# Kernel optimization log

Measured on AMD Instinct MI355X. Metric: run time of the kernel, lower is better.

## Reference

```python
import jax, jax.numpy as jnp
import numpy as np

B, S, HID = 8, 4096, 1024
NH, HD = 16, 64  # heads, head_dim
LN_EPS = 1e-12


def setup_inputs() -> dict:
    key = jax.random.key(0)
    ks = jax.random.split(key, 12)
    sd = 1.0 / np.sqrt(HID)
    return {
        "input_tensor": jax.random.normal(ks[0], (B, S, HID), jnp.float32),
        "attention_mask": jnp.ones((B, S), jnp.int32),
        "ln_gamma": jnp.ones((HID,), jnp.float32),
        "ln_beta": jnp.zeros((HID,), jnp.float32),
        "Wq": jax.random.normal(ks[1], (HID, HID), jnp.float32) * sd,
        "bq": jnp.zeros((HID,), jnp.float32),
        "Wk": jax.random.normal(ks[2], (HID, HID), jnp.float32) * sd,
        "bk": jnp.zeros((HID,), jnp.float32),
        "Wv": jax.random.normal(ks[3], (HID, HID), jnp.float32) * sd,
        "bv": jnp.zeros((HID,), jnp.float32),
        "Wo": jax.random.normal(ks[4], (HID, HID), jnp.float32) * sd,
        "bo": jnp.zeros((HID,), jnp.float32),
    }


def _layernorm(x, g, b):
    mu = jnp.mean(x, axis=-1, keepdims=True)
    var = jnp.mean(jnp.square(x - mu), axis=-1, keepdims=True)
    return (x - mu) * jax.lax.rsqrt(var + LN_EPS) * g + b


def reference(input_tensor, attention_mask, ln_gamma, ln_beta,
              Wq, bq, Wk, bk, Wv, bv, Wo, bo):
    # NOTE: attention_mask is accepted but unused, matching the original module.
    x = input_tensor
    x_norm = _layernorm(x, ln_gamma, ln_beta)
    # projections: query from normalized input, key/value from raw input
    q = (x_norm @ Wq.T + bq).reshape(B, S, NH, HD).transpose(0, 2, 1, 3)  # bhsd
    k = (x @ Wk.T + bk).reshape(B, S, NH, HD).transpose(0, 2, 1, 3)      # bhsd
    v = (x @ Wv.T + bv).reshape(B, S, NH, HD).transpose(0, 2, 1, 3)      # bhsd

    eq = jax.nn.elu(q)
    ek = jax.nn.elu(k)
    # per-token L2 norms over head_dim (matches norm over d in both layouts)
    eq = eq / jnp.linalg.norm(eq, axis=-1, keepdims=True)
    ek = ek / jnp.linalg.norm(ek, axis=-1, keepdims=True)

    # linear attention: Q (K^T V), never materializing [S,S]
    kv = jnp.einsum('bhsd,bhse->bhde', ek, v)          # [B,H,d,d]
    ctx = jnp.einsum('bhsd,bhde->bhse', eq, kv) / np.sqrt(HD)

    ctx = ctx.transpose(0, 2, 1, 3).reshape(B, S, HID)
    out = ctx @ Wo.T + bo
    return out + x  # residual (dropouts are identity in eval mode)
```

## Files before the change

kernel.cpp:

```cpp
#include <hip/hip_runtime.h>

typedef unsigned short u16;
typedef unsigned int   u32;
typedef __attribute__((ext_vector_type(8))) __bf16 bf16x8;
typedef __attribute__((ext_vector_type(4))) float  f32x4;

#define BQ   8
#define SQ   4096
#define NHQ  16
#define HIDD 1024
#define TOKN 32768

__device__ __forceinline__ u16 f2bf(float f){
  u32 u = __builtin_bit_cast(u32, f);
  u += 0x7fffu + ((u >> 16) & 1u);
  return (u16)(u >> 16);
}
__device__ __forceinline__ float bf2f(u16 h){
  return __builtin_bit_cast(float, (u32)h << 16);
}
__device__ __forceinline__ void gl16(const void* g, void* l){
  __builtin_amdgcn_global_load_lds((const __attribute__((address_space(1))) void*)g,
                                   (__attribute__((address_space(3))) void*)l, 16, 0, 0);
}
#define MFMA(a,b,c) __builtin_amdgcn_mfma_f32_16x16x32_bf16((a),(b),(c),0,0,0)

__global__ __launch_bounds__(256) void k_cast4(const float* __restrict__ wq,
    const float* __restrict__ wk, const float* __restrict__ wv, const float* __restrict__ wo,
    u16* __restrict__ oq, u16* __restrict__ okv, u16* __restrict__ oo){
  const int sel = blockIdx.x >> 10;
  const int i = ((blockIdx.x & 1023) << 8) + threadIdx.x;
  const float* in = (sel == 0) ? wq : (sel == 1) ? wk : (sel == 2) ? wv : wo;
  u16* o = (sel == 0) ? oq : (sel == 1) ? okv : (sel == 2) ? (okv + 1024 * 1024) : oo;
  float4 v = ((const float4*)in)[i];
  ushort4 r;
  r.x = f2bf(v.x); r.y = f2bf(v.y); r.z = f2bf(v.z); r.w = f2bf(v.w);
  ((ushort4*)o)[i] = r;
}

__global__ __launch_bounds__(256) void k_ln(const float* __restrict__ x, const float* __restrict__ g,
    const float* __restrict__ be, u16* __restrict__ xbf, u16* __restrict__ xnbf){
  const int row = blockIdx.x, t = threadIdx.x;
  const float4 v = ((const float4*)(x + (size_t)row * HIDD))[t];
  float s  = v.x + v.y + v.z + v.w;
  float ss = v.x*v.x + v.y*v.y + v.z*v.z + v.w*v.w;
  #pragma unroll
  for (int o = 1; o < 64; o <<= 1){ s += __shfl_xor(s, o); ss += __shfl_xor(ss, o); }
  __shared__ float sm[8];
  const int lane = t & 63, wid = t >> 6;
  if (lane == 0){ sm[wid] = s; sm[wid + 4] = ss; }
  __syncthreads();
  s  = sm[0] + sm[1] + sm[2] + sm[3];
  ss = sm[4] + sm[5] + sm[6] + sm[7];
  const float mu   = s * (1.f / 1024.f);
  const float var  = ss * (1.f / 1024.f) - mu * mu;
  const float rstd = rsqrtf(var + 1e-12f);
  const float4 gg = ((const float4*)g)[t];
  const float4 bb = ((const float4*)be)[t];
  ushort4 xo, no;
  xo.x = f2bf(v.x); no.x = f2bf((v.x - mu) * rstd * gg.x + bb.x);
  xo.y = f2bf(v.y); no.y = f2bf((v.y - mu) * rstd * gg.y + bb.y);
  xo.z = f2bf(v.z); no.z = f2bf((v.z - mu) * rstd * gg.z + bb.z);
  xo.w = f2bf(v.w); no.w = f2bf((v.w - mu) * rstd * gg.w + bb.w);
  ((ushort4*)(xbf  + (size_t)row * HIDD))[t] = xo;
  ((ushort4*)(xnbf + (size_t)row * HIDD))[t] = no;
}

struct GP {
  const u16* A; const u16* W; const float* b1; const float* b2;
  int nsplit, lgNB, LDC, nblk; u16* outb;
};

template<int RES>
__global__ __launch_bounds__(512, 2) void k_gemm256(GP p0, GP p1, int seg0,
    const float* __restrict__ resid, float* __restrict__ outf){
  __shared__ union {
    u16 st[2][2][16384];
    float cep[8][1056];
  } sm;

  const GP& p = (blockIdx.x < seg0) ? p0 : p1;
  const int bseg = (blockIdx.x < seg0) ? blockIdx.x : blockIdx.x - seg0;
  const u16* __restrict__ A = p.A;
  const u16* __restrict__ W = p.W;
  const int lgNB = p.lgNB, LDC = p.LDC;

  const int wg = ((bseg & 7) * (p.nblk >> 3)) + (bseg >> 3);
  const int m0 = (wg >> lgNB) << 8;
  const int n0 = (wg & ((1 << lgNB) - 1)) << 8;

  const int t = threadIdx.x, lane = t & 63, wid = t >> 6;
  const int ln15 = lane & 15, hi = lane >> 4;
  const int wr = wid >> 2, wc = wid & 3;
  const int lg = lane & 7, lr = lane >> 3;

  auto stage = [&](int buf, int op, const u16* __restrict__ src, int rowoff, int kt){
    #pragma unroll
    for (int i = 0; i < 4; i++){
      const int cb  = ((i << 3) + wid) << 6;
      const int row = (cb >> 3) + lr;
      const int g   = lg ^ lr;
      gl16(src + (size_t)(rowoff + row) * HIDD + (kt << 6) + (g << 3),
           &sm.st[buf][op][cb << 3]);
    }
  };
  #define RD_A(c,m,ks) (*(const bf16x8*)&sm.st[c][0][(((wr << 7) + ((m) << 4) + ln15) << 6) + \
      (((((ks) << 2) + hi) ^ (lane & 7)) << 3)])
  #define RD_B(c,n,ks) (*(const bf16x8*)&sm.st[c][1][(((wc << 6) + ((n) << 4) + ln15) << 6) + \
      (((((ks) << 2) + hi) ^ (lane & 7)) << 3)])

  f32x4 acc[8][4] = {};

  stage(0, 0, A, m0, 0);
  stage(0, 1, W, n0, 0);
  stage(1, 1, W, n0, 1);
  asm volatile("s_waitcnt vmcnt(4)" ::: "memory");
  __builtin_amdgcn_s_barrier();
  asm volatile("" ::: "memory");

  const int NT = HIDD / 64;
  for (int kt = 0; kt < NT; ++kt){
    const int c = kt & 1;
    bf16x8 af[4][2], bq[4][2];
    #pragma unroll
    for (int m = 0; m < 4; m++){ af[m][0] = RD_A(c, m, 0); af[m][1] = RD_A(c, m, 1); }
    #pragma unroll
    for (int n = 0; n < 4; n++){ bq[n][0] = RD_B(c, n, 0); bq[n][1] = RD_B(c, n, 1); }
    const int ka = kt + 1 < NT ? kt + 1 : NT - 1;
    stage(c ^ 1, 0, A, m0, ka);
    __builtin_amdgcn_s_setprio(1);
    #pragma unroll
    for (int m = 0; m < 4; m++)
      #pragma unroll
      for (int n = 0; n < 4; n++){
        acc[m][n] = MFMA(af[m][0], bq[n][0], acc[m][n]);
        acc[m][n] = MFMA(af[m][1], bq[n][1], acc[m][n]);
      }
    __builtin_amdgcn_s_setprio(0);
    asm volatile("" ::: "memory");
    __builtin_amdgcn_s_barrier();
    asm volatile("" ::: "memory");
    #pragma unroll
    for (int m = 0; m < 4; m++){ af[m][0] = RD_A(c, m + 4, 0); af[m][1] = RD_A(c, m + 4, 1); }
    const int kb = kt + 2 < NT ? kt + 2 : NT - 1;
    stage(c, 1, W, n0, kb);
    __builtin_amdgcn_s_setprio(1);
    #pragma unroll
    for (int m = 0; m < 4; m++)
      #pragma unroll
      for (int n = 0; n < 4; n++){
        acc[m + 4][n] = MFMA(af[m][0], bq[n][0], acc[m + 4][n]);
        acc[m + 4][n] = MFMA(af[m][1], bq[n][1], acc[m + 4][n]);
      }
    __builtin_amdgcn_s_setprio(0);
    asm volatile("s_waitcnt vmcnt(4)" ::: "memory");
    __builtin_amdgcn_s_barrier();
    asm volatile("" ::: "memory");
  }
  #undef RD_A
  #undef RD_B

  asm volatile("s_waitcnt vmcnt(0)" ::: "memory");
  __builtin_amdgcn_s_barrier();
  asm volatile("" ::: "memory");

  const float* bp = (n0 < p.nsplit) ? p.b1 : (p.b2 - p.nsplit);
  float bn[4];
  #pragma unroll
  for (int n = 0; n < 4; n++) bn[n] = bp[n0 + (wc << 6) + (n << 4) + ln15];

  float* cw = &sm.cep[wid][0];
  const int rr = lane >> 3, cb8 = (lane & 7) << 3;

  if constexpr (RES){
    #pragma unroll
    for (int m = 0; m < 8; m++){
      #pragma unroll
      for (int n = 0; n < 4; n++)
        #pragma unroll
        for (int r = 0; r < 4; r++)
          cw[((hi << 2) + r) * 66 + (n << 4) + ln15] = acc[m][n][r] + bn[n];
      #pragma unroll
      for (int j = 0; j < 2; j++){
        const int row = (j << 3) + rr;
        const size_t gr = (size_t)(m0 + (wr << 7) + (m << 4) + row);
        const size_t gidx = gr * LDC + n0 + (wc << 6) + cb8;
        const size_t ridx = gr * HIDD + n0 + (wc << 6) + cb8;
        const float4 ra = *(const float4*)&resid[ridx];
        const float4 rb = *(const float4*)&resid[ridx + 4];
        float4 o0, o1;
        o0.x = cw[row * 66 + cb8 + 0] + ra.x;
        o0.y = cw[row * 66 + cb8 + 1] + ra.y;
        o0.z = cw[row * 66 + cb8 + 2] + ra.z;
        o0.w = cw[row * 66 + cb8 + 3] + ra.w;
        o1.x = cw[row * 66 + cb8 + 4] + rb.x;
        o1.y = cw[row * 66 + cb8 + 5] + rb.y;
        o1.z = cw[row * 66 + cb8 + 6] + rb.z;
        o1.w = cw[row * 66 + cb8 + 7] + rb.w;
        *(float4*)&outf[gidx]     = o0;
        *(float4*)&outf[gidx + 4] = o1;
      }
    }
  } else {
    u16* outb = p.outb;
    #pragma unroll
    for (int m = 0; m < 8; m++){
      #pragma unroll
      for (int n = 0; n < 4; n++)
        #pragma unroll
        for (int r = 0; r < 4; r++)
          cw[((hi << 2) + r) * 66 + (n << 4) + ln15] = acc[m][n][r] + bn[n];
      #pragma unroll
      for (int j = 0; j < 2; j++){
        const int row = (j << 3) + rr;
        u32 ro[4];
        #pragma unroll
        for (int pq = 0; pq < 4; pq++){
          float v0 = cw[row * 66 + cb8 + 2 * pq];
          float v1 = cw[row * 66 + cb8 + 2 * pq + 1];
          ro[pq] = (u32)f2bf(v0) | ((u32)f2bf(v1) << 16);
        }
        uint4 o; o.x = ro[0]; o.y = ro[1]; o.z = ro[2]; o.w = ro[3];
        *(uint4*)&outb[(size_t)(m0 + (wr << 7) + (m << 4) + row) * LDC
                       + n0 + (wc << 6) + cb8] = o;
      }
    }
  }
}

__global__ __launch_bounds__(256) void k_transpose2(const u16* __restrict__ kvb,
                                                    u16* __restrict__ ekT, u16* __restrict__ vT){
  __shared__ float tile[64][65];
  __shared__ float pr[64][4];
  __shared__ float rn[64];
  const int sb = blockIdx.x << 6, h2 = blockIdx.y, b = blockIdx.z;
  const int h = h2 & 15;
  const int isK = (h2 >> 4) == 0;
  const u16* in = kvb + ((h2 >> 4) << 10);
  u16* outp = isK ? ekT : vT;
  const int t = threadIdx.x;
  {
    const int tok = t >> 2, q = t & 3;
    const u16* src = in + (size_t)(b * SQ + sb + tok) * 2048 + (h << 6) + (q << 4);
    uint4 u0 = *(const uint4*)src;
    uint4 u1 = *(const uint4*)(src + 8);
    u32 uu[8] = {u0.x, u0.y, u0.z, u0.w, u1.x, u1.y, u1.z, u1.w};
    float ss = 0.f;
    #pragma unroll
    for (int i = 0; i < 8; i++){
      float f0 = bf2f((u16)(uu[i] & 0xffff));
      float f1 = bf2f((u16)(uu[i] >> 16));
      if (isK){
        f0 = f0 > 0.f ? f0 : expm1f(f0);
        f1 = f1 > 0.f ? f1 : expm1f(f1);
        ss += f0 * f0 + f1 * f1;
      }
      tile[tok][(q << 4) + 2*i]     = f0;
      tile[tok][(q << 4) + 2*i + 1] = f1;
    }
    if (isK) pr[tok][q] = ss;
  }
  __syncthreads();
  if (isK){
    if (t < 64) rn[t] = rsqrtf(pr[t][0] + pr[t][1] + pr[t][2] + pr[t][3]);
    __syncthreads();
  }
  const int d = t >> 2, sq2 = (t & 3) << 4;
  u16* dst = outp + ((size_t)(b * NHQ + h) * 64 + d) * SQ + sb + sq2;
  u32 ro[8];
  #pragma unroll
  for (int i = 0; i < 8; i++){
    float v0 = tile[sq2 + 2*i][d];
    float v1 = tile[sq2 + 2*i + 1][d];
    if (isK){ v0 *= rn[sq2 + 2*i]; v1 *= rn[sq2 + 2*i + 1]; }
    ro[i] = (u32)f2bf(v0) | ((u32)f2bf(v1) << 16);
  }
  uint4 o0; o0.x = ro[0]; o0.y = ro[1]; o0.z = ro[2]; o0.w = ro[3];
  uint4 o1; o1.x = ro[4]; o1.y = ro[5]; o1.z = ro[6]; o1.w = ro[7];
  *(uint4*)dst = o0;
  *(uint4*)(dst + 8) = o1;
}

__global__ __launch_bounds__(256) void k_kv(const u16* __restrict__ vT, const u16* __restrict__ ekT,
                                            u16* __restrict__ kvT){
  const int bh = blockIdx.x;
  const u16* Av = vT  + (size_t)bh * 64 * SQ;
  const u16* Bk = ekT + (size_t)bh * 64 * SQ;
  const int lane = threadIdx.x & 63, wid = threadIdx.x >> 6;
  const int ln15 = lane & 15, hi = lane >> 4;
  f32x4 acc[4][4] = {};
  const int kb = wid << 10;
  for (int ks = 0; ks < 32; ++ks){
    const int k0 = kb + (ks << 5) + (hi << 3);
    bf16x8 af[4], bfr[4];
    #pragma unroll
    for (int m = 0; m < 4; m++) af[m]  = *(const bf16x8*)(Av + (size_t)((m << 4) + ln15) * SQ + k0);
    #pragma unroll
    for (int n = 0; n < 4; n++) bfr[n] = *(const bf16x8*)(Bk + (size_t)((n << 4) + ln15) * SQ + k0);
    #pragma unroll
    for (int m = 0; m < 4; m++)
      #pragma unroll
      for (int n = 0; n < 4; n++)
        acc[m][n] = MFMA(af[m], bfr[n], acc[m][n]);
  }
  __shared__ float red[64][64];
  for (int w = 0; w < 4; ++w){
    if (wid == w){
      #pragma unroll
      for (int m = 0; m < 4; m++)
        #pragma unroll
        for (int n = 0; n < 4; n++)
          #pragma unroll
          for (int r = 0; r < 4; r++){
            int row = (m << 4) + (hi << 2) + r;
            int col = (n << 4) + ln15;
            if (w == 0) red[row][col] = acc[m][n][r];
            else        red[row][col] += acc[m][n][r];
          }
    }
    __syncthreads();
  }
  u16* dst = kvT + (size_t)bh * 4096;
  const int tt = threadIdx.x;
  #pragma unroll
  for (int i = 0; i < 16; i++){
    int idx = tt * 16 + i;
    dst[idx] = f2bf(red[idx >> 6][idx & 63] * 0.125f);
  }
}

__global__ __launch_bounds__(256) void k_ctx(const u16* __restrict__ q, const u16* __restrict__ kvT,
                                             u16* __restrict__ ctx){
  __shared__ u16 Alds[1024 * 8];
  __shared__ u16 Blds[512 * 8];
  __shared__ float prn[128][2];
  const int sb = blockIdx.x << 7;
  const int h = blockIdx.y, b = blockIdx.z;
  const int bh = (b << 4) + h;
  const int t = threadIdx.x, lane = t & 63, wid = t >> 6;
  const int ln15 = lane & 15, hi = lane >> 4;
  {
    uint4 va[4]; uint4 vb[2];
    #pragma unroll
    for (int i = 0; i < 4; i++){
      int c = (wid << 6) + (i << 8) + lane;
      int g = c >> 7, row = c & 127;
      va[i] = *(const uint4*)(q + (size_t)(b * SQ + sb + row) * HIDD + (h << 6) + g * 8);
    }
    #pragma unroll
    for (int i = 0; i < 2; i++){
      int c = (wid << 6) + (i << 8) + lane;
      int g = c >> 6, row = c & 63;
      vb[i] = *(const uint4*)(kvT + (size_t)bh * 4096 + (row << 6) + g * 8);
    }
    #pragma unroll
    for (int i = 0; i < 4; i++)
      *(uint4*)&Alds[((wid << 6) + (i << 8) + lane) * 8] = va[i];
    #pragma unroll
    for (int i = 0; i < 2; i++)
      *(uint4*)&Blds[((wid << 6) + (i << 8) + lane) * 8] = vb[i];
  }
  __syncthreads();
  {
    const int row = t & 127, half = t >> 7;
    float vals[4][8]; float ss = 0.f;
    #pragma unroll
    for (int g4 = 0; g4 < 4; g4++){
      const int g = (half << 2) + g4;
      uint4 u = *(const uint4*)&Alds[((g << 7) + row) * 8];
      u32 uu[4] = {u.x, u.y, u.z, u.w};
      #pragma unroll
      for (int i = 0; i < 4; i++){
        float f0 = bf2f((u16)(uu[i] & 0xffff));
        float f1 = bf2f((u16)(uu[i] >> 16));
        f0 = f0 > 0.f ? f0 : expm1f(f0);
        f1 = f1 > 0.f ? f1 : expm1f(f1);
        vals[g4][2*i] = f0; vals[g4][2*i+1] = f1;
        ss += f0 * f0 + f1 * f1;
      }
    }
    prn[row][half] = ss;
    __syncthreads();
    const float rn = rsqrtf(prn[row][0] + prn[row][1]);
    #pragma unroll
    for (int g4 = 0; g4 < 4; g4++){
      const int g = (half << 2) + g4;
      u32 ro[4];
      #pragma unroll
      for (int i = 0; i < 4; i++)
        ro[i] = (u32)f2bf(vals[g4][2*i] * rn) | ((u32)f2bf(vals[g4][2*i+1] * rn) << 16);
      uint4 o; o.x = ro[0]; o.y = ro[1]; o.z = ro[2]; o.w = ro[3];
      *(uint4*)&Alds[((g << 7) + row) * 8] = o;
    }
  }
  __syncthreads();
  f32x4 acc[2][4] = {};
  #pragma unroll
  for (int k2 = 0; k2 < 2; k2++){
    const int g = (k2 << 2) + hi;
    bf16x8 af[2], bfr[4];
    #pragma unroll
    for (int m = 0; m < 2; m++) af[m]  = *(const bf16x8*)&Alds[((g << 7) + (wid << 5) + (m << 4) + ln15) * 8];
    #pragma unroll
    for (int n = 0; n < 4; n++) bfr[n] = *(const bf16x8*)&Blds[((g << 6) + (n << 4) + ln15) * 8];
    #pragma unroll
    for (int m = 0; m < 2; m++)
      #pragma unroll
      for (int n = 0; n < 4; n++)
        acc[m][n] = MFMA(af[m], bfr[n], acc[m][n]);
  }
  #pragma unroll
  for (int m = 0; m < 2; m++)
    #pragma unroll
    for (int n = 0; n < 4; n++)
      #pragma unroll
      for (int r = 0; r < 4; r++){
        int srow = sb + (wid << 5) + (m << 4) + (hi << 2) + r;
        int col  = (n << 4) + ln15;
        ctx[(size_t)(b * SQ + srow) * HIDD + (h << 6) + col] = f2bf(acc[m][n][r]);
      }
}

extern "C" void kernel_launch(void* const* d_in, const int* in_sizes, int n_in,
                              void* d_out, int out_size, void* d_ws, size_t ws_size,
                              hipStream_t stream){
  const float* x   = (const float*)d_in[0];
  const float* lng = (const float*)d_in[2];
  const float* lnb = (const float*)d_in[3];
  const float* Wq  = (const float*)d_in[4];
  const float* bq  = (const float*)d_in[5];
  const float* Wk  = (const float*)d_in[6];
  const float* bk  = (const float*)d_in[7];
  const float* Wv  = (const float*)d_in[8];
  const float* bv  = (const float*)d_in[9];
  const float* Wo  = (const float*)d_in[10];
  const float* bo  = (const float*)d_in[11];
  float* out = (float*)d_out;

  char* w = (char*)d_ws;
  const size_t MB = 1ull << 20;
  u16* wqb  = (u16*)(w + 0   * MB);
  u16* wkvb = (u16*)(w + 2   * MB);
  u16* wob  = (u16*)(w + 6   * MB);
  u16* xbf  = (u16*)(w + 8   * MB);
  u16* xnbf = (u16*)(w + 72  * MB);
  u16* qb   = (u16*)(w + 136 * MB);
  u16* kvb  = (u16*)(w + 200 * MB);
  u16* kvT  = (u16*)(w + 328 * MB);
  u16* ekT = xnbf;
  u16* vT  = xbf;
  u16* ctx = kvb;

  k_cast4<<<4096, 256, 0, stream>>>(Wq, Wk, Wv, Wo, wqb, wkvb, wob);
  k_ln<<<TOKN, 256, 0, stream>>>(x, lng, lnb, xbf, xnbf);

  GP pq  = { xnbf, wqb,  bq, bq, 1 << 30, 2, 1024, 512,  qb  };
  GP pkv = { xbf,  wkvb, bk, bv, 1024,    3, 2048, 1024, kvb };
  k_gemm256<0><<<1536, 512, 0, stream>>>(pq, pkv, 512, nullptr, nullptr);

  k_transpose2<<<dim3(64, 32, 8), 256, 0, stream>>>(kvb, ekT, vT);
  k_kv<<<128, 256, 0, stream>>>(vT, ekT, kvT);
  k_ctx<<<dim3(32, 16, 8), 256, 0, stream>>>(qb, kvT, ctx);

  GP po = { ctx, wob, bo, bo, 1 << 30, 2, 1024, 512, nullptr };
  k_gemm256<1><<<512, 512, 0, stream>>>(po, po, 512, x, out);

  (void)in_sizes; (void)n_in; (void)out_size; (void)ws_size;
}
```

Measured before the change: 693.0 us.

## Write V transposed from QKV GEMM epilogue and split output GEMM pipeline finer

The QKV GEMM epilogue now writes the V half directly in transposed [b,h,d,s] layout, so the separate transpose kernel only handles K (elu plus normalize). This drops one full read and write of V through global memory. The output-projection GEMM also switches to a variant that issues A/B staging in quarter steps, with four barriers per k-tile instead of two. That adds synchronization overhead in exchange for interleaving loads more finely with MFMA work.

```diff
diff --git a/kernel.cpp b/kernel.cpp
--- a/kernel.cpp
+++ b/kernel.cpp
@@ -68,15 +68,16 @@
 
 struct GP {
   const u16* A; const u16* W; const float* b1; const float* b2;
-  int nsplit, lgNB, LDC, nblk; u16* outb;
+  int nsplit, lgNB, LDC, nblk; u16* outb; u16* voutT;
 };
 
-template<int RES>
+template<int RES, int SPLIT>
 __global__ __launch_bounds__(512, 2) void k_gemm256(GP p0, GP p1, int seg0,
     const float* __restrict__ resid, float* __restrict__ outf){
   __shared__ union {
     u16 st[2][2][16384];
     float cep[8][1056];
+    float cep2[8][2112];
   } sm;
 
   const GP& p = (blockIdx.x < seg0) ? p0 : p1;
@@ -104,10 +105,22 @@
            &sm.st[buf][op][cb << 3]);
     }
   };
+  auto stageH = [&](int buf, int op, const u16* __restrict__ src, int rowoff, int kt, int half){
+    #pragma unroll
+    for (int i2 = 0; i2 < 2; i2++){
+      const int i = (half << 1) + i2;
+      const int cb  = ((i << 3) + wid) << 6;
+      const int row = (cb >> 3) + lr;
+      const int g   = lg ^ lr;
+      gl16(src + (size_t)(rowoff + row) * HIDD + (kt << 6) + (g << 3),
+           &sm.st[buf][op][cb << 3]);
+    }
+  };
   #define RD_A(c,m,ks) (*(const bf16x8*)&sm.st[c][0][(((wr << 7) + ((m) << 4) + ln15) << 6) + \
       (((((ks) << 2) + hi) ^ (lane & 7)) << 3)])
   #define RD_B(c,n,ks) (*(const bf16x8*)&sm.st[c][1][(((wc << 6) + ((n) << 4) + ln15) << 6) + \
       (((((ks) << 2) + hi) ^ (lane & 7)) << 3)])
+  #define BARF do { asm volatile("" ::: "memory"); __builtin_amdgcn_s_barrier(); asm volatile("" ::: "memory"); } while(0)
 
   f32x4 acc[8][4] = {};
 
@@ -115,64 +128,122 @@
   stage(0, 1, W, n0, 0);
   stage(1, 1, W, n0, 1);
   asm volatile("s_waitcnt vmcnt(4)" ::: "memory");
-  __builtin_amdgcn_s_barrier();
-  asm volatile("" ::: "memory");
+  BARF;
 
   const int NT = HIDD / 64;
-  for (int kt = 0; kt < NT; ++kt){
-    const int c = kt & 1;
-    bf16x8 af[4][2], bq[4][2];
-    #pragma unroll
-    for (int m = 0; m < 4; m++){ af[m][0] = RD_A(c, m, 0); af[m][1] = RD_A(c, m, 1); }
-    #pragma unroll
-    for (int n = 0; n < 4; n++){ bq[n][0] = RD_B(c, n, 0); bq[n][1] = RD_B(c, n, 1); }
-    const int ka = kt + 1 < NT ? kt + 1 : NT - 1;
-    stage(c ^ 1, 0, A, m0, ka);
-    __builtin_amdgcn_s_setprio(1);
-    #pragma unroll
-    for (int m = 0; m < 4; m++)
-      #pragma unroll
-      for (int n = 0; n < 4; n++){
-        acc[m][n] = MFMA(af[m][0], bq[n][0], acc[m][n]);
-        acc[m][n] = MFMA(af[m][1], bq[n][1], acc[m][n]);
-      }
-    __builtin_amdgcn_s_setprio(0);
-    asm volatile("" ::: "memory");
-    __builtin_amdgcn_s_barrier();
-    asm volatile("" ::: "memory");
-    #pragma unroll
-    for (int m = 0; m < 4; m++){ af[m][0] = RD_A(c, m + 4, 0); af[m][1] = RD_A(c, m + 4, 1); }
-    const int kb = kt + 2 < NT ? kt + 2 : NT - 1;
-    stage(c, 1, W, n0, kb);
-    __builtin_amdgcn_s_setprio(1);
-    #pragma unroll
-    for (int m = 0; m < 4; m++)
-      #pragma unroll
-      for (int n = 0; n < 4; n++){
-        acc[m + 4][n] = MFMA(af[m][0], bq[n][0], acc[m + 4][n]);
-        acc[m + 4][n] = MFMA(af[m][1], bq[n][1], acc[m + 4][n]);
-      }
-    __builtin_amdgcn_s_setprio(0);
-    asm volatile("s_waitcnt vmcnt(4)" ::: "memory");
-    __builtin_amdgcn_s_barrier();
-    asm volatile("" ::: "memory");
+  if constexpr (SPLIT == 0){
+    for (int kt = 0; kt < NT; ++kt){
+      const int c = kt & 1;
+      bf16x8 af[4][2], bq[4][2];
+      #pragma unroll
+      for (int m = 0; m < 4; m++){ af[m][0] = RD_A(c, m, 0); af[m][1] = RD_A(c, m, 1); }
+      #pragma unroll
+      for (int n = 0; n < 4; n++){ bq[n][0] = RD_B(c, n, 0); bq[n][1] = RD_B(c, n, 1); }
+      const int ka = kt + 1 < NT ? kt + 1 : NT - 1;
+      stage(c ^ 1, 0, A, m0, ka);
+      __builtin_amdgcn_s_setprio(1);
+      #pragma unroll
+      for (int m = 0; m < 4; m++)
+        #pragma unroll
+        for (int n = 0; n < 4; n++){
+          acc[m][n] = MFMA(af[m][0], bq[n][0], acc[m][n]);
+          acc[m][n] = MFMA(af[m][1], bq[n][1], acc[m][n]);
+        }
+      __builtin_amdgcn_s_setprio(0);
+      BARF;
+      #pragma unroll
+      for (int m = 0; m < 4; m++){ af[m][0] = RD_A(c, m + 4, 0); af[m][1] = RD_A(c, m + 4, 1); }
+      const int kb = kt + 2 < NT ? kt + 2 : NT - 1;
+      stage(c, 1, W, n0, kb);
+      __builtin_amdgcn_s_setprio(1);
+      #pragma unroll
+      for (int m = 0; m < 4; m++)
+        #pragma unroll
+        for (int n = 0; n < 4; n++){
+          acc[m + 4][n] = MFMA(af[m][0], bq[n][0], acc[m + 4][n]);
+          acc[m + 4][n] = MFMA(af[m][1], bq[n][1], acc[m + 4][n]);
+        }
+      __builtin_amdgcn_s_setprio(0);
+      asm volatile("s_waitcnt vmcnt(4)" ::: "memory");
+      BARF;
+    }
+  } else {
+    for (int kt = 0; kt < NT; ++kt){
+      const int c = kt & 1;
+      const int ka  = kt + 1 < NT ? kt + 1 : NT - 1;
+      const int kb2 = kt + 2 < NT ? kt + 2 : NT - 1;
+      bf16x8 af[2][2], bq[4][2];
+      af[0][0] = RD_A(c, 0, 0); af[0][1] = RD_A(c, 0, 1);
+      af[1][0] = RD_A(c, 1, 0); af[1][1] = RD_A(c, 1, 1);
+      #pragma unroll
+      for (int n = 0; n < 4; n++){ bq[n][0] = RD_B(c, n, 0); bq[n][1] = RD_B(c, n, 1); }
+      stageH(c ^ 1, 0, A, m0, ka, 0);
+      __builtin_amdgcn_s_setprio(1);
+      #pragma unroll
+      for (int m = 0; m < 2; m++)
+        #pragma unroll
+        for (int n = 0; n < 4; n++){
+          acc[m][n] = MFMA(af[m][0], bq[n][0], acc[m][n]);
+          acc[m][n] = MFMA(af[m][1], bq[n][1], acc[m][n]);
+        }
+      __builtin_amdgcn_s_setprio(0);
+      BARF;
+      af[0][0] = RD_A(c, 2, 0); af[0][1] = RD_A(c, 2, 1);
+      af[1][0] = RD_A(c, 3, 0); af[1][1] = RD_A(c, 3, 1);
+      stageH(c ^ 1, 0, A, m0, ka, 1);
+      __builtin_amdgcn_s_setprio(1);
+      #pragma unroll
+      for (int m = 0; m < 2; m++)
+        #pragma unroll
+        for (int n = 0; n < 4; n++){
+          acc[m + 2][n] = MFMA(af[m][0], bq[n][0], acc[m + 2][n]);
+          acc[m + 2][n] = MFMA(af[m][1], bq[n][1], acc[m + 2][n]);
+        }
+      __builtin_amdgcn_s_setprio(0);
+      BARF;
+      af[0][0] = RD_A(c, 4, 0); af[0][1] = RD_A(c, 4, 1);
+      af[1][0] = RD_A(c, 5, 0); af[1][1] = RD_A(c, 5, 1);
+      stageH(c, 1, W, n0, kb2, 0);
+      __builtin_amdgcn_s_setprio(1);
+      #pragma unroll
+      for (int m = 0; m < 2; m++)
+        #pragma unroll
+        for (int n = 0; n < 4; n++){
+          acc[m + 4][n] = MFMA(af[m][0], bq[n][0], acc[m + 4][n]);
+          acc[m + 4][n] = MFMA(af[m][1], bq[n][1], acc[m + 4][n]);
+        }
+      __builtin_amdgcn_s_setprio(0);
+      BARF;
+      af[0][0] = RD_A(c, 6, 0); af[0][1] = RD_A(c, 6, 1);
+      af[1][0] = RD_A(c, 7, 0); af[1][1] = RD_A(c, 7, 1);
+      stageH(c, 1, W, n0, kb2, 1);
+      __builtin_amdgcn_s_setprio(1);
+      #pragma unroll
+      for (int m = 0; m < 2; m++)
+        #pragma unroll
+        for (int n = 0; n < 4; n++){
+          acc[m + 6][n] = MFMA(af[m][0], bq[n][0], acc[m + 6][n]);
+          acc[m + 6][n] = MFMA(af[m][1], bq[n][1], acc[m + 6][n]);
+        }
+      __builtin_amdgcn_s_setprio(0);
+      asm volatile("s_waitcnt vmcnt(4)" ::: "memory");
+      BARF;
+    }
   }
   #undef RD_A
   #undef RD_B
 
   asm volatile("s_waitcnt vmcnt(0)" ::: "memory");
-  __builtin_amdgcn_s_barrier();
-  asm volatile("" ::: "memory");
+  BARF;
 
   const float* bp = (n0 < p.nsplit) ? p.b1 : (p.b2 - p.nsplit);
   float bn[4];
   #pragma unroll
   for (int n = 0; n < 4; n++) bn[n] = bp[n0 + (wc << 6) + (n << 4) + ln15];
 
-  float* cw = &sm.cep[wid][0];
-  const int rr = lane >> 3, cb8 = (lane & 7) << 3;
-
   if constexpr (RES){
+    float* cw = &sm.cep[wid][0];
+    const int rr = lane >> 3, cb8 = (lane & 7) << 3;
     #pragma unroll
     for (int m = 0; m < 8; m++){
       #pragma unroll
@@ -201,7 +272,41 @@
         *(float4*)&outf[gidx + 4] = o1;
       }
     }
+  } else if (p.voutT != nullptr && n0 >= p.nsplit){
+    float* cw = &sm.cep2[wid][0];
+    const int e0 = n0 - p.nsplit + (wc << 6);
+    const int hh = e0 >> 6;
+    u16* vt = p.voutT;
+    #pragma unroll
+    for (int mp = 0; mp < 4; mp++){
+      #pragma unroll
+      for (int mh = 0; mh < 2; mh++){
+        const int m = (mp << 1) + mh;
+        #pragma unroll
+        for (int n = 0; n < 4; n++)
+          #pragma unroll
+          for (int r = 0; r < 4; r++)
+            cw[((mh << 4) + (hi << 2) + r) * 66 + (n << 4) + ln15] = acc[m][n][r] + bn[n];
+      }
+      const int rg0 = m0 + (wr << 7) + (mp << 5);
+      const int bb = rg0 >> 12, s0 = rg0 & 4095;
+      u16* dst = vt + (((size_t)(bb << 4) + hh) * 64 + lane) * SQ + s0;
+      #pragma unroll
+      for (int j = 0; j < 4; j++){
+        u32 ro[4];
+        #pragma unroll
+        for (int q = 0; q < 4; q++){
+          float v0 = cw[((j << 3) + 2 * q    ) * 66 + lane];
+          float v1 = cw[((j << 3) + 2 * q + 1) * 66 + lane];
+          ro[q] = (u32)f2bf(v0) | ((u32)f2bf(v1) << 16);
+        }
+        uint4 o; o.x = ro[0]; o.y = ro[1]; o.z = ro[2]; o.w = ro[3];
+        *(uint4*)&dst[j << 3] = o;
+      }
+    }
   } else {
+    float* cw = &sm.cep[wid][0];
+    const int rr = lane >> 3, cb8 = (lane & 7) << 3;
     u16* outb = p.outb;
     #pragma unroll
     for (int m = 0; m < 8; m++){
@@ -226,22 +331,19 @@
       }
     }
   }
-}
-
-__global__ __launch_bounds__(256) void k_transpose2(const u16* __restrict__ kvb,
-                                                    u16* __restrict__ ekT, u16* __restrict__ vT){
+  #undef BARF
+}
+
+__global__ __launch_bounds__(256) void k_transposeK(const u16* __restrict__ kb,
+                                                    u16* __restrict__ ekT){
   __shared__ float tile[64][65];
   __shared__ float pr[64][4];
   __shared__ float rn[64];
-  const int sb = blockIdx.x << 6, h2 = blockIdx.y, b = blockIdx.z;
-  const int h = h2 & 15;
-  const int isK = (h2 >> 4) == 0;
-  const u16* in = kvb + ((h2 >> 4) << 10);
-  u16* outp = isK ? ekT : vT;
+  const int sb = blockIdx.x << 6, h = blockIdx.y, b = blockIdx.z;
   const int t = threadIdx.x;
   {
     const int tok = t >> 2, q = t & 3;
-    const u16* src = in + (size_t)(b * SQ + sb + tok) * 2048 + (h << 6) + (q << 4);
+    const u16* src = kb + (size_t)(b * SQ + sb + tok) * 1024 + (h << 6) + (q << 4);
     uint4 u0 = *(const uint4*)src;
     uint4 u1 = *(const uint4*)(src + 8);
     u32 uu[8] = {u0.x, u0.y, u0.z, u0.w, u1.x, u1.y, u1.z, u1.w};
@@ -250,29 +352,24 @@
     for (int i = 0; i < 8; i++){
       float f0 = bf2f((u16)(uu[i] & 0xffff));
       float f1 = bf2f((u16)(uu[i] >> 16));
-      if (isK){
-        f0 = f0 > 0.f ? f0 : expm1f(f0);
-        f1 = f1 > 0.f ? f1 : expm1f(f1);
-        ss += f0 * f0 + f1 * f1;
-      }
+      f0 = f0 > 0.f ? f0 : expm1f(f0);
+      f1 = f1 > 0.f ? f1 : expm1f(f1);
+      ss += f0 * f0 + f1 * f1;
       tile[tok][(q << 4) + 2*i]     = f0;
       tile[tok][(q << 4) + 2*i + 1] = f1;
     }
-    if (isK) pr[tok][q] = ss;
+    pr[tok][q] = ss;
   }
   __syncthreads();
-  if (isK){
-    if (t < 64) rn[t] = rsqrtf(pr[t][0] + pr[t][1] + pr[t][2] + pr[t][3]);
-    __syncthreads();
-  }
+  if (t < 64) rn[t] = rsqrtf(pr[t][0] + pr[t][1] + pr[t][2] + pr[t][3]);
+  __syncthreads();
   const int d = t >> 2, sq2 = (t & 3) << 4;
-  u16* dst = outp + ((size_t)(b * NHQ + h) * 64 + d) * SQ + sb + sq2;
+  u16* dst = ekT + ((size_t)(b * NHQ + h) * 64 + d) * SQ + sb + sq2;
   u32 ro[8];
   #pragma unroll
   for (int i = 0; i < 8; i++){
-    float v0 = tile[sq2 + 2*i][d];
-    float v1 = tile[sq2 + 2*i + 1][d];
-    if (isK){ v0 *= rn[sq2 + 2*i]; v1 *= rn[sq2 + 2*i + 1]; }
+    float v0 = tile[sq2 + 2*i][d]     * rn[sq2 + 2*i];
+    float v1 = tile[sq2 + 2*i + 1][d] * rn[sq2 + 2*i + 1];
     ro[i] = (u32)f2bf(v0) | ((u32)f2bf(v1) << 16);
   }
   uint4 o0; o0.x = ro[0]; o0.y = ro[1]; o0.z = ro[2]; o0.w = ro[3];
@@ -445,25 +542,25 @@
   u16* xbf  = (u16*)(w + 8   * MB);
   u16* xnbf = (u16*)(w + 72  * MB);
   u16* qb   = (u16*)(w + 136 * MB);
-  u16* kvb  = (u16*)(w + 200 * MB);
+  u16* kb   = (u16*)(w + 200 * MB);
+  u16* vT   = (u16*)(w + 264 * MB);
   u16* kvT  = (u16*)(w + 328 * MB);
   u16* ekT = xnbf;
-  u16* vT  = xbf;
-  u16* ctx = kvb;
+  u16* ctx = kb;
 
   k_cast4<<<4096, 256, 0, stream>>>(Wq, Wk, Wv, Wo, wqb, wkvb, wob);
   k_ln<<<TOKN, 256, 0, stream>>>(x, lng, lnb, xbf, xnbf);
 
-  GP pq  = { xnbf, wqb,  bq, bq, 1 << 30, 2, 1024, 512,  qb  };
-  GP pkv = { xbf,  wkvb, bk, bv, 1024,    3, 2048, 1024, kvb };
-  k_gemm256<0><<<1536, 512, 0, stream>>>(pq, pkv, 512, nullptr, nullptr);
-
-  k_transpose2<<<dim3(64, 32, 8), 256, 0, stream>>>(kvb, ekT, vT);
+  GP pq  = { xnbf, wqb,  bq, bq, 1 << 30, 2, 1024, 512,  qb, nullptr };
+  GP pkv = { xbf,  wkvb, bk, bv, 1024,    3, 1024, 1024, kb, vT };
+  k_gemm256<0, 0><<<1536, 512, 0, stream>>>(pq, pkv, 512, nullptr, nullptr);
+
+  k_transposeK<<<dim3(64, 16, 8), 256, 0, stream>>>(kb, ekT);
   k_kv<<<128, 256, 0, stream>>>(vT, ekT, kvT);
   k_ctx<<<dim3(32, 16, 8), 256, 0, stream>>>(qb, kvT, ctx);
 
-  GP po = { ctx, wob, bo, bo, 1 << 30, 2, 1024, 512, nullptr };
-  k_gemm256<1><<<512, 512, 0, stream>>>(po, po, 512, x, out);
+  GP po = { ctx, wob, bo, bo, 1 << 30, 2, 1024, 512, nullptr, nullptr };
+  k_gemm256<1, 1><<<512, 512, 0, stream>>>(po, po, 512, x, out);
 
   (void)in_sizes; (void)n_in; (void)out_size; (void)ws_size;
 }
```

New measurement: 685.8 us. Within noise of the previous version (-1.0%).

## Fuse ELU/L2-norm into QKV GEMM epilogue and fold KV into output weights

Applied to the files above, without the earlier changes.

The Q/K/V GEMM epilogue now applies ELU and per-head L2 normalization directly and writes K and V transposed per head, which removes the separate transpose kernel. The ctx kernel is gone: a new kernel multiplies each batch-head's KV matrix into Wo to form a per-batch effective weight, and the output GEMM then reads normalized Q against that batch-specific weight. This drops the ctx intermediate and two launches, but the final GEMM now loads a different weight per batch, and the epilogue does extra shuffles and expm1 work.

```diff
diff --git a/kernel.cpp b/kernel.cpp
--- a/kernel.cpp
+++ b/kernel.cpp
@@ -68,7 +68,7 @@
 
 struct GP {
   const u16* A; const u16* W; const float* b1; const float* b2;
-  int nsplit, lgNB, LDC, nblk; u16* outb;
+  int nsplit, eluN, lgNB, LDC, nblk, wPerBatch; u16* outb; u16* koutT; u16* voutT;
 };
 
 template<int RES>
@@ -77,17 +77,19 @@
   __shared__ union {
     u16 st[2][2][16384];
     float cep[8][1056];
+    float cep2[8][2112];
   } sm;
 
   const GP& p = (blockIdx.x < seg0) ? p0 : p1;
   const int bseg = (blockIdx.x < seg0) ? blockIdx.x : blockIdx.x - seg0;
-  const u16* __restrict__ A = p.A;
-  const u16* __restrict__ W = p.W;
   const int lgNB = p.lgNB, LDC = p.LDC;
 
   const int wg = ((bseg & 7) * (p.nblk >> 3)) + (bseg >> 3);
   const int m0 = (wg >> lgNB) << 8;
   const int n0 = (wg & ((1 << lgNB) - 1)) << 8;
+
+  const u16* __restrict__ A = p.A;
+  const u16* __restrict__ W = p.W + (p.wPerBatch ? ((size_t)(m0 >> 12) << 20) : 0);
 
   const int t = threadIdx.x, lane = t & 63, wid = t >> 6;
   const int ln15 = lane & 15, hi = lane >> 4;
@@ -108,6 +110,7 @@
       (((((ks) << 2) + hi) ^ (lane & 7)) << 3)])
   #define RD_B(c,n,ks) (*(const bf16x8*)&sm.st[c][1][(((wc << 6) + ((n) << 4) + ln15) << 6) + \
       (((((ks) << 2) + hi) ^ (lane & 7)) << 3)])
+  #define BARF do { asm volatile("" ::: "memory"); __builtin_amdgcn_s_barrier(); asm volatile("" ::: "memory"); } while(0)
 
   f32x4 acc[8][4] = {};
 
@@ -115,8 +118,7 @@
   stage(0, 1, W, n0, 0);
   stage(1, 1, W, n0, 1);
   asm volatile("s_waitcnt vmcnt(4)" ::: "memory");
-  __builtin_amdgcn_s_barrier();
-  asm volatile("" ::: "memory");
+  BARF;
 
   const int NT = HIDD / 64;
   for (int kt = 0; kt < NT; ++kt){
@@ -137,9 +139,7 @@
         acc[m][n] = MFMA(af[m][1], bq[n][1], acc[m][n]);
       }
     __builtin_amdgcn_s_setprio(0);
-    asm volatile("" ::: "memory");
-    __builtin_amdgcn_s_barrier();
-    asm volatile("" ::: "memory");
+    BARF;
     #pragma unroll
     for (int m = 0; m < 4; m++){ af[m][0] = RD_A(c, m + 4, 0); af[m][1] = RD_A(c, m + 4, 1); }
     const int kb = kt + 2 < NT ? kt + 2 : NT - 1;
@@ -154,25 +154,39 @@
       }
     __builtin_amdgcn_s_setprio(0);
     asm volatile("s_waitcnt vmcnt(4)" ::: "memory");
-    __builtin_amdgcn_s_barrier();
-    asm volatile("" ::: "memory");
+    BARF;
   }
   #undef RD_A
   #undef RD_B
 
   asm volatile("s_waitcnt vmcnt(0)" ::: "memory");
-  __builtin_amdgcn_s_barrier();
-  asm volatile("" ::: "memory");
+  BARF;
 
   const float* bp = (n0 < p.nsplit) ? p.b1 : (p.b2 - p.nsplit);
   float bn[4];
   #pragma unroll
   for (int n = 0; n < 4; n++) bn[n] = bp[n0 + (wc << 6) + (n << 4) + ln15];
-
-  float* cw = &sm.cep[wid][0];
-  const int rr = lane >> 3, cb8 = (lane & 7) << 3;
+  const bool elu = (n0 < p.eluN);
+
+  auto rowvals = [&](int m, int r, float* e){
+    float s2 = 0.f;
+    #pragma unroll
+    for (int n = 0; n < 4; n++){
+      float v = acc[m][n][r] + bn[n];
+      if (elu){ v = v > 0.f ? v : expm1f(v); s2 += v * v; }
+      e[n] = v;
+    }
+    if (elu){
+      s2 += __shfl_xor(s2, 1); s2 += __shfl_xor(s2, 2);
+      s2 += __shfl_xor(s2, 4); s2 += __shfl_xor(s2, 8);
+      const float rf = rsqrtf(s2);
+      e[0] *= rf; e[1] *= rf; e[2] *= rf; e[3] *= rf;
+    }
+  };
 
   if constexpr (RES){
+    float* cw = &sm.cep[wid][0];
+    const int rr = lane >> 3, cb8 = (lane & 7) << 3;
     #pragma unroll
     for (int m = 0; m < 8; m++){
       #pragma unroll
@@ -201,15 +215,56 @@
         *(float4*)&outf[gidx + 4] = o1;
       }
     }
+  } else if (p.koutT != nullptr){
+    float* cw = &sm.cep2[wid][0];
+    const int isK = (n0 < p.nsplit);
+    const int cb = (isK ? n0 : n0 - p.nsplit) + (wc << 6);
+    const int hh = cb >> 6;
+    u16* vt = isK ? p.koutT : p.voutT;
+    #pragma unroll
+    for (int mp = 0; mp < 4; mp++){
+      #pragma unroll
+      for (int mh = 0; mh < 2; mh++){
+        const int m = (mp << 1) + mh;
+        #pragma unroll
+        for (int r = 0; r < 4; r++){
+          float e[4];
+          rowvals(m, r, e);
+          #pragma unroll
+          for (int n = 0; n < 4; n++)
+            cw[((mh << 4) + (hi << 2) + r) * 66 + (n << 4) + ln15] = e[n];
+        }
+      }
+      const int rg0 = m0 + (wr << 7) + (mp << 5);
+      const int bb = rg0 >> 12, s0 = rg0 & 4095;
+      u16* dst = vt + (((size_t)(bb << 4) + hh) * 64 + lane) * SQ + s0;
+      #pragma unroll
+      for (int j = 0; j < 4; j++){
+        u32 ro[4];
+        #pragma unroll
+        for (int q = 0; q < 4; q++){
+          float v0 = cw[((j << 3) + 2 * q    ) * 66 + lane];
+          float v1 = cw[((j << 3) + 2 * q + 1) * 66 + lane];
+          ro[q] = (u32)f2bf(v0) | ((u32)f2bf(v1) << 16);
+        }
+        uint4 o; o.x = ro[0]; o.y = ro[1]; o.z = ro[2]; o.w = ro[3];
+        *(uint4*)&dst[j << 3] = o;
+      }
+    }
   } else {
+    float* cw = &sm.cep[wid][0];
+    const int rr = lane >> 3, cb8 = (lane & 7) << 3;
     u16* outb = p.outb;
     #pragma unroll
     for (int m = 0; m < 8; m++){
       #pragma unroll
-      for (int n = 0; n < 4; n++)
-        #pragma unroll
-        for (int r = 0; r < 4; r++)
-          cw[((hi << 2) + r) * 66 + (n << 4) + ln15] = acc[m][n][r] + bn[n];
+      for (int r = 0; r < 4; r++){
+        float e[4];
+        rowvals(m, r, e);
+        #pragma unroll
+        for (int n = 0; n < 4; n++)
+          cw[((hi << 2) + r) * 66 + (n << 4) + ln15] = e[n];
+      }
       #pragma unroll
       for (int j = 0; j < 2; j++){
         const int row = (j << 3) + rr;
@@ -226,63 +281,11 @@
       }
     }
   }
-}
-
-__global__ __launch_bounds__(256) void k_transpose2(const u16* __restrict__ kvb,
-                                                    u16* __restrict__ ekT, u16* __restrict__ vT){
-  __shared__ float tile[64][65];
-  __shared__ float pr[64][4];
-  __shared__ float rn[64];
-  const int sb = blockIdx.x << 6, h2 = blockIdx.y, b = blockIdx.z;
-  const int h = h2 & 15;
-  const int isK = (h2 >> 4) == 0;
-  const u16* in = kvb + ((h2 >> 4) << 10);
-  u16* outp = isK ? ekT : vT;
-  const int t = threadIdx.x;
-  {
-    const int tok = t >> 2, q = t & 3;
-    const u16* src = in + (size_t)(b * SQ + sb + tok) * 2048 + (h << 6) + (q << 4);
-    uint4 u0 = *(const uint4*)src;
-    uint4 u1 = *(const uint4*)(src + 8);
-    u32 uu[8] = {u0.x, u0.y, u0.z, u0.w, u1.x, u1.y, u1.z, u1.w};
-    float ss = 0.f;
-    #pragma unroll
-    for (int i = 0; i < 8; i++){
-      float f0 = bf2f((u16)(uu[i] & 0xffff));
-      float f1 = bf2f((u16)(uu[i] >> 16));
-      if (isK){
-        f0 = f0 > 0.f ? f0 : expm1f(f0);
-        f1 = f1 > 0.f ? f1 : expm1f(f1);
-        ss += f0 * f0 + f1 * f1;
-      }
-      tile[tok][(q << 4) + 2*i]     = f0;
-      tile[tok][(q << 4) + 2*i + 1] = f1;
-    }
-    if (isK) pr[tok][q] = ss;
-  }
-  __syncthreads();
-  if (isK){
-    if (t < 64) rn[t] = rsqrtf(pr[t][0] + pr[t][1] + pr[t][2] + pr[t][3]);
-    __syncthreads();
-  }
-  const int d = t >> 2, sq2 = (t & 3) << 4;
-  u16* dst = outp + ((size_t)(b * NHQ + h) * 64 + d) * SQ + sb + sq2;
-  u32 ro[8];
-  #pragma unroll
-  for (int i = 0; i < 8; i++){
-    float v0 = tile[sq2 + 2*i][d];
-    float v1 = tile[sq2 + 2*i + 1][d];
-    if (isK){ v0 *= rn[sq2 + 2*i]; v1 *= rn[sq2 + 2*i + 1]; }
-    ro[i] = (u32)f2bf(v0) | ((u32)f2bf(v1) << 16);
-  }
-  uint4 o0; o0.x = ro[0]; o0.y = ro[1]; o0.z = ro[2]; o0.w = ro[3];
-  uint4 o1; o1.x = ro[4]; o1.y = ro[5]; o1.z = ro[6]; o1.w = ro[7];
-  *(uint4*)dst = o0;
-  *(uint4*)(dst + 8) = o1;
+  #undef BARF
 }
 
 __global__ __launch_bounds__(256) void k_kv(const u16* __restrict__ vT, const u16* __restrict__ ekT,
-                                            u16* __restrict__ kvT){
+                                            u16* __restrict__ kvF){
   const int bh = blockIdx.x;
   const u16* Av = vT  + (size_t)bh * 64 * SQ;
   const u16* Bk = ekT + (size_t)bh * 64 * SQ;
@@ -320,105 +323,52 @@
     }
     __syncthreads();
   }
-  u16* dst = kvT + (size_t)bh * 4096;
+  u16* dst = kvF + (size_t)bh * 4096;
   const int tt = threadIdx.x;
   #pragma unroll
   for (int i = 0; i < 16; i++){
     int idx = tt * 16 + i;
-    dst[idx] = f2bf(red[idx >> 6][idx & 63] * 0.125f);
-  }
-}
-
-__global__ __launch_bounds__(256) void k_ctx(const u16* __restrict__ q, const u16* __restrict__ kvT,
-                                             u16* __restrict__ ctx){
-  __shared__ u16 Alds[1024 * 8];
-  __shared__ u16 Blds[512 * 8];
-  __shared__ float prn[128][2];
-  const int sb = blockIdx.x << 7;
-  const int h = blockIdx.y, b = blockIdx.z;
-  const int bh = (b << 4) + h;
+    dst[idx] = f2bf(red[idx & 63][idx >> 6] * 0.125f);
+  }
+}
+
+__global__ __launch_bounds__(256) void k_mb(const u16* __restrict__ kvF,
+    const u16* __restrict__ wob, u16* __restrict__ Mb){
+  __shared__ u16 stg[4][64][72];
+  const int j0 = blockIdx.x << 8, bh = blockIdx.y;
+  const int b = bh >> 4, h = bh & 15;
   const int t = threadIdx.x, lane = t & 63, wid = t >> 6;
   const int ln15 = lane & 15, hi = lane >> 4;
-  {
-    uint4 va[4]; uint4 vb[2];
-    #pragma unroll
-    for (int i = 0; i < 4; i++){
-      int c = (wid << 6) + (i << 8) + lane;
-      int g = c >> 7, row = c & 127;
-      va[i] = *(const uint4*)(q + (size_t)(b * SQ + sb + row) * HIDD + (h << 6) + g * 8);
-    }
-    #pragma unroll
-    for (int i = 0; i < 2; i++){
-      int c = (wid << 6) + (i << 8) + lane;
-      int g = c >> 6, row = c & 63;
-      vb[i] = *(const uint4*)(kvT + (size_t)bh * 4096 + (row << 6) + g * 8);
-    }
-    #pragma unroll
-    for (int i = 0; i < 4; i++)
-      *(uint4*)&Alds[((wid << 6) + (i << 8) + lane) * 8] = va[i];
-    #pragma unroll
-    for (int i = 0; i < 2; i++)
-      *(uint4*)&Blds[((wid << 6) + (i << 8) + lane) * 8] = vb[i];
-  }
-  __syncthreads();
-  {
-    const int row = t & 127, half = t >> 7;
-    float vals[4][8]; float ss = 0.f;
-    #pragma unroll
-    for (int g4 = 0; g4 < 4; g4++){
-      const int g = (half << 2) + g4;
-      uint4 u = *(const uint4*)&Alds[((g << 7) + row) * 8];
-      u32 uu[4] = {u.x, u.y, u.z, u.w};
-      #pragma unroll
-      for (int i = 0; i < 4; i++){
-        float f0 = bf2f((u16)(uu[i] & 0xffff));
-        float f1 = bf2f((u16)(uu[i] >> 16));
-        f0 = f0 > 0.f ? f0 : expm1f(f0);
-        f1 = f1 > 0.f ? f1 : expm1f(f1);
-        vals[g4][2*i] = f0; vals[g4][2*i+1] = f1;
-        ss += f0 * f0 + f1 * f1;
-      }
-    }
-    prn[row][half] = ss;
-    __syncthreads();
-    const float rn = rsqrtf(prn[row][0] + prn[row][1]);
-    #pragma unroll
-    for (int g4 = 0; g4 < 4; g4++){
-      const int g = (half << 2) + g4;
-      u32 ro[4];
-      #pragma unroll
-      for (int i = 0; i < 4; i++)
-        ro[i] = (u32)f2bf(vals[g4][2*i] * rn) | ((u32)f2bf(vals[g4][2*i+1] * rn) << 16);
-      uint4 o; o.x = ro[0]; o.y = ro[1]; o.z = ro[2]; o.w = ro[3];
-      *(uint4*)&Alds[((g << 7) + row) * 8] = o;
-    }
-  }
-  __syncthreads();
-  f32x4 acc[2][4] = {};
-  #pragma unroll
-  for (int k2 = 0; k2 < 2; k2++){
-    const int g = (k2 << 2) + hi;
-    bf16x8 af[2], bfr[4];
-    #pragma unroll
-    for (int m = 0; m < 2; m++) af[m]  = *(const bf16x8*)&Alds[((g << 7) + (wid << 5) + (m << 4) + ln15) * 8];
-    #pragma unroll
-    for (int n = 0; n < 4; n++) bfr[n] = *(const bf16x8*)&Blds[((g << 6) + (n << 4) + ln15) * 8];
-    #pragma unroll
-    for (int m = 0; m < 2; m++)
+  const u16* Ak = kvF + (size_t)bh * 4096;
+  f32x4 acc[4][4] = {};
+  #pragma unroll
+  for (int ks = 0; ks < 2; ++ks){
+    bf16x8 af[4], bfr[4];
+    #pragma unroll
+    for (int m = 0; m < 4; m++)
+      af[m] = *(const bf16x8*)(wob + (size_t)(j0 + (wid << 6) + (m << 4) + ln15) * 1024
+                                + (h << 6) + (ks << 5) + (hi << 3));
+    #pragma unroll
+    for (int n = 0; n < 4; n++)
+      bfr[n] = *(const bf16x8*)(Ak + (((n << 4) + ln15) << 6) + (ks << 5) + (hi << 3));
+    #pragma unroll
+    for (int m = 0; m < 4; m++)
       #pragma unroll
       for (int n = 0; n < 4; n++)
         acc[m][n] = MFMA(af[m], bfr[n], acc[m][n]);
   }
   #pragma unroll
-  for (int m = 0; m < 2; m++)
+  for (int m = 0; m < 4; m++)
     #pragma unroll
     for (int n = 0; n < 4; n++)
       #pragma unroll
-      for (int r = 0; r < 4; r++){
-        int srow = sb + (wid << 5) + (m << 4) + (hi << 2) + r;
-        int col  = (n << 4) + ln15;
-        ctx[(size_t)(b * SQ + srow) * HIDD + (h << 6) + col] = f2bf(acc[m][n][r]);
-      }
+      for (int r = 0; r < 4; r++)
+        stg[wid][(m << 4) + (hi << 2) + r][(n << 4) + ln15] = f2bf(acc[m][n][r]);
+  __syncthreads();
+  u16* dst = Mb + ((size_t)b << 20) + (size_t)(j0 + (wid << 6) + lane) * 1024 + (h << 6);
+  #pragma unroll
+  for (int q = 0; q < 8; ++q)
+    *(uint4*)&dst[q << 3] = *(const uint4*)&stg[wid][lane][q << 3];
 }
 
 extern "C" void kernel_launch(void* const* d_in, const int* in_sizes, int n_in,
@@ -445,24 +395,22 @@
   u16* xbf  = (u16*)(w + 8   * MB);
   u16* xnbf = (u16*)(w + 72  * MB);
   u16* qb   = (u16*)(w + 136 * MB);
-  u16* kvb  = (u16*)(w + 200 * MB);
-  u16* kvT  = (u16*)(w + 328 * MB);
-  u16* ekT = xnbf;
-  u16* vT  = xbf;
-  u16* ctx = kvb;
+  u16* ekT  = (u16*)(w + 200 * MB);
+  u16* vT   = (u16*)(w + 264 * MB);
+  u16* kvF  = (u16*)(w + 328 * MB);
+  u16* Mb   = xbf;
 
   k_cast4<<<4096, 256, 0, stream>>>(Wq, Wk, Wv, Wo, wqb, wkvb, wob);
   k_ln<<<TOKN, 256, 0, stream>>>(x, lng, lnb, xbf, xnbf);
 
-  GP pq  = { xnbf, wqb,  bq, bq, 1 << 30, 2, 1024, 512,  qb  };
-  GP pkv = { xbf,  wkvb, bk, bv, 1024,    3, 2048, 1024, kvb };
+  GP pq  = { xnbf, wqb,  bq, bq, 1 << 30, 1 << 30, 2, 1024, 512,  0, qb,      nullptr, nullptr };
+  GP pkv = { xbf,  wkvb, bk, bv, 1024,    1024,    3, 1024, 1024, 0, nullptr, ekT,     vT      };
   k_gemm256<0><<<1536, 512, 0, stream>>>(pq, pkv, 512, nullptr, nullptr);
 
-  k_transpose2<<<dim3(64, 32, 8), 256, 0, stream>>>(kvb, ekT, vT);
-  k_kv<<<128, 256, 0, stream>>>(vT, ekT, kvT);
-  k_ctx<<<dim3(32, 16, 8), 256, 0, stream>>>(qb, kvT, ctx);
-
-  GP po = { ctx, wob, bo, bo, 1 << 30, 2, 1024, 512, nullptr };
+  k_kv<<<128, 256, 0, stream>>>(vT, ekT, kvF);
+  k_mb<<<dim3(4, 128), 256, 0, stream>>>(kvF, wob, Mb);
+
+  GP po = { qb, Mb, bo, bo, 1 << 30, 0, 2, 1024, 512, 1, nullptr, nullptr, nullptr };
   k_gemm256<1><<<512, 512, 0, stream>>>(po, po, 512, x, out);
 
   (void)in_sizes; (void)n_in; (void)out_size; (void)ws_size;
```

Result: slower. 717.7 us (+3.6%).
